# Kernel tuning notes

Hardware: AMD Instinct MI355X
Metric: run time of the kernel (lower is better)

Reference implementation:

```python
import jax, jax.numpy as jnp
import numpy as np

N, E, H = 5000, 40000, 8
DIMS = [(258, 512), (516, 256), (262, 128), (136, 20)]  # (in_feature, out_feature) per GATDeformer


def setup_inputs() -> dict:
    key = jax.random.key(0)
    ks = jax.random.split(key, 10)
    s = 0.05
    data = jax.random.normal(ks[0], (N, 10), jnp.float32)
    src = jax.random.randint(ks[1], (E,), 0, N)
    off = jax.random.randint(ks[2], (E,), 1, N)
    edge_idx = jnp.stack([src, (src + off) % N]).astype(jnp.int32)  # no self loops by construction
    inp = {
        'data': data,
        'edge_idx': edge_idx,
        'W0': jax.random.normal(ks[3], (10, 256), jnp.float32) * s,
        'b0': jnp.zeros((256,), jnp.float32),
    }
    for i, (din, dout) in enumerate(DIMS, start=1):
        k = jax.random.split(ks[3 + i], 3)
        inp[f'W{i}'] = jax.random.normal(k[0], (din, H * dout), jnp.float32) * s
        inp[f'asrc{i}'] = jax.random.normal(k[1], (H, dout), jnp.float32) * s
        inp[f'adst{i}'] = jax.random.normal(k[2], (H, dout), jnp.float32) * s
        inp[f'bias{i}'] = jnp.zeros((dout,), jnp.float32)
    return inp


def _gat(x, src, dst, W, a_s, a_d, b):
    """PyG GATConv (concat=False): returns (mean-over-heads output + bias, alpha [E',H])."""
    Hh, C = a_s.shape
    h = (x @ W).reshape(N, Hh, C)                               # [N,H,C]
    e_s = jnp.einsum('nhc,hc->nh', h, a_s)                      # [N,H]
    e_d = jnp.einsum('nhc,hc->nh', h, a_d)
    logits = jax.nn.leaky_relu(e_s[src] + e_d[dst], 0.2)        # [E',H]
    m = jax.ops.segment_max(logits, dst, num_segments=N)        # segment softmax over incoming edges
    ex = jnp.exp(logits - m[dst])
    alpha = ex / jax.ops.segment_sum(ex, dst, num_segments=N)[dst]
    out = jax.ops.segment_sum(alpha[:, :, None] * h[src], dst, num_segments=N)  # [N,H,C]
    return out.mean(axis=1) + b, alpha


def _deformer(af, src, dst, W, a_s, a_d, b):
    # find_boundary on the layer input features
    up, down = af[:, 0] == 1.0, af[:, 0] == 0.0
    left, right = af[:, 1] == 0.0, af[:, 1] == 1.0
    feat, alpha = _gat(af, src, dst, W, a_s, a_d, b)
    coord = af[:, :2]
    # second propagate: alpha*0.2 reused to aggregate source coordinates, then mean over heads
    msg = (alpha * 0.2)[:, :, None] * coord[src][:, None, :]    # [E',H,2]
    oc = jax.ops.segment_sum(msg, dst, num_segments=N).mean(axis=1)
    # fix_boundary (sequential overwrite order: up then down, left then right)
    c0 = jnp.where(down, 0.0, jnp.where(up, 1.0, oc[:, 0]))
    c1 = jnp.where(right, 1.0, jnp.where(left, 0.0, oc[:, 1]))
    return jnp.stack([c0, c1], axis=1), jax.nn.selu(feat)


def reference(data, edge_idx, W0, b0, W1, asrc1, adst1, bias1, W2, asrc2, adst2, bias2, W3, asrc3, adst3, bias3, W4, asrc4, adst4, bias4):
    sl = jnp.arange(N, dtype=edge_idx.dtype)
    src = jnp.concatenate([edge_idx[0], sl])   # GATConv add_self_loops=True
    dst = jnp.concatenate([edge_idx[1], sl])
    coord = data[:, :2]
    feat = jax.nn.selu(data @ W0 + b0)
    c1_, f1 = _deformer(jnp.concatenate([coord, feat], 1), src, dst, W1, asrc1, adst1, bias1)
    c2_, f2 = _deformer(jnp.concatenate([c1_, coord, f1], 1), src, dst, W2, asrc2, adst2, bias2)
    c3_, f3 = _deformer(jnp.concatenate([c2_, c1_, coord, f2], 1), src, dst, W3, asrc3, adst3, bias3)
    c4_, _ = _deformer(jnp.concatenate([c3_, c2_, c1_, coord, f3], 1), src, dst, W4, asrc4, adst4, bias4)
    return c4_
```

## Files before the change

### kernel.cpp

```cpp
#include <hip/hip_runtime.h>

#define N_NODES 5000
#define NH 8

typedef unsigned short u16;
typedef short bf16x8 __attribute__((ext_vector_type(8)));
typedef float f32x4 __attribute__((ext_vector_type(4)));

static __device__ __forceinline__ float selu_f(float x) {
    const float sc = 1.0507009873554805f;
    const float al = 1.6732632423543772f;
    return x > 0.f ? sc * x : sc * al * (__expf(x) - 1.f);
}

static __device__ __forceinline__ u16 f2bf(float x) {
    union { float f; unsigned u; } v; v.f = x;
    unsigned r = v.u + 0x7fff + ((v.u >> 16) & 1);
    return (u16)(r >> 16);
}

static __device__ __forceinline__ float bf2f(unsigned hi16) {
    union { unsigned u; float f; } v; v.u = hi16 << 16;
    return v.f;
}

#define GL2LDS16(gp, lp)                                                        \
    __builtin_amdgcn_global_load_lds(                                           \
        (const __attribute__((address_space(1))) void*)(gp),                    \
        (__attribute__((address_space(3))) void*)(lp), 16, 0, 0)

#define WAVE_LDS_FENCE() asm volatile("s_waitcnt lgkmcnt(0)" ::: "memory")

__global__ void k_count(const int* __restrict__ ei, int* cnt, int E, int Esz) {
    int e = blockIdx.x * 256 + threadIdx.x;
    if (e >= Esz) return;
    int dst = (e < E) ? ei[E + e] : (e - E);
    atomicAdd(&cnt[dst], 1);
}

__global__ void k_scan(const int* __restrict__ cnt, int* __restrict__ rowp, int n) {
    __shared__ int ps[256];
    int t = threadIdx.x;
    int per = (n + 255) / 256;
    int b = t * per;
    int s = 0;
    for (int i = 0; i < per; ++i) { int idx = b + i; if (idx < n) s += cnt[idx]; }
    ps[t] = s;
    __syncthreads();
    for (int off = 1; off < 256; off <<= 1) {
        int v = (t >= off) ? ps[t - off] : 0;
        __syncthreads();
        ps[t] += v;
        __syncthreads();
    }
    int run = (t == 0) ? 0 : ps[t - 1];
    for (int i = 0; i < per; ++i) {
        int idx = b + i;
        if (idx < n) { rowp[idx] = run; run += cnt[idx]; }
    }
    if (t == 255) rowp[n] = run;
}

__global__ void k_fill(const int* __restrict__ ei, const int* __restrict__ rowp,
                       int* cur, int* ssrc, int E, int Esz) {
    int e = blockIdx.x * 256 + threadIdx.x;
    if (e >= Esz) return;
    int src, dst;
    if (e < E) { src = ei[e]; dst = ei[E + e]; }
    else       { src = e - E; dst = src; }
    int pos = rowp[dst] + atomicAdd(&cur[dst], 1);
    ssrc[pos] = src;
}

__global__ __launch_bounds__(256) void k_prep(
        const float* W1, const float* W2, const float* W3, const float* W4,
        const float* s1, const float* s2, const float* s3, const float* s4,
        const float* d1, const float* d2, const float* d3, const float* d4,
        float* __restrict__ fsAll, float* __restrict__ fdAll,
        u16* T1, u16* T2, u16* T3) {
    const int Ks[4] = {258, 516, 262, 136};
    const int Cs[4] = {512, 256, 128, 20};
    int bid = blockIdx.x;
    if (bid < 516) {
        int li = bid / 129;
        int k = (bid % 129) * 4 + (threadIdx.x >> 6);
        int lane = threadIdx.x & 63;
        if (k >= Ks[li]) return;
        const float* W  = (li == 0) ? W1 : (li == 1) ? W2 : (li == 2) ? W3 : W4;
        const float* as = (li == 0) ? s1 : (li == 1) ? s2 : (li == 2) ? s3 : s4;
        const float* ad = (li == 0) ? d1 : (li == 1) ? d2 : (li == 2) ? d3 : d4;
        int C = Cs[li];
        float s[8] = {0.f,0.f,0.f,0.f,0.f,0.f,0.f,0.f};
        float d[8] = {0.f,0.f,0.f,0.f,0.f,0.f,0.f,0.f};
        const float* wr = W + (size_t)k * 8 * C;
        for (int c = lane; c < C; c += 64) {
            #pragma unroll
            for (int h = 0; h < 8; ++h) {
                float w = wr[h * C + c];
                s[h] += w * as[h * C + c];
                d[h] += w * ad[h * C + c];
            }
        }
        #pragma unroll
        for (int off = 32; off >= 1; off >>= 1) {
            #pragma unroll
            for (int h = 0; h < 8; ++h) {
                s[h] += __shfl_xor(s[h], off);
                d[h] += __shfl_xor(d[h], off);
            }
        }
        if (lane == 0) {
            float* fo = fsAll + (size_t)li * 516 * 8 + k * 8;
            float* go = fdAll + (size_t)li * 516 * 8 + k * 8;
            #pragma unroll
            for (int h = 0; h < 8; ++h) { fo[h] = s[h]; go[h] = d[h]; }
        }
    } else {
        const int Kps[3] = {288, 544, 288};
        int w = bid - 516;
        int li = w / (16 * 136);
        int rem = w % (16 * 136);
        int c0 = (rem % 16) * 32;
        int j0 = (rem / 16) * 32;
        int C = Cs[li], K = Ks[li], Kp = Kps[li], KK = 8 * Kp;
        if (c0 >= C || j0 >= KK) return;
        const float* W = (li == 0) ? W1 : (li == 1) ? W2 : W3;
        u16* Wt2 = (li == 0) ? T1 : (li == 1) ? T2 : T3;
        __shared__ float tile[32][33];
        int h = j0 / Kp, k0 = j0 % Kp;
        int tid = threadIdx.x;
        for (int idx = tid; idx < 1024; idx += 256) {
            int kr = idx >> 5, cc = idx & 31;
            int gk = k0 + kr;
            tile[kr][cc] = (gk < K) ? W[(size_t)gk * (8 * C) + h * C + c0 + cc] : 0.f;
        }
        __syncthreads();
        for (int idx = tid; idx < 1024; idx += 256) {
            int cr = idx >> 5, kc = idx & 31;
            Wt2[(size_t)(c0 + cr) * KK + j0 + kc] = f2bf(tile[kc][cr]);
        }
    }
}

__global__ __launch_bounds__(256) void k_mf(const float* p0, const float* p1,
                                            const float* p2, const float* p3, int np,
                                            const float* __restrict__ data,
                                            const float* __restrict__ W0,
                                            const float* __restrict__ b0,
                                            const u16* __restrict__ facc,
                                            const float* __restrict__ biasp,
                                            int split, int MN, int FC, int K, int Kp,
                                            const float* __restrict__ fs,
                                            const float* __restrict__ fd,
                                            u16* __restrict__ afb,
                                            float* __restrict__ es, float* __restrict__ ed,
                                            float* __restrict__ c0out) {
    int n = blockIdx.x, t = threadIdx.x;
    __shared__ float drow[10];
    bool l1 = (biasp == nullptr);
    if (l1 && t < 10) drow[t] = data[n * 10 + t];
    __syncthreads();
    float pes[8] = {0.f,0.f,0.f,0.f,0.f,0.f,0.f,0.f};
    float ped[8] = {0.f,0.f,0.f,0.f,0.f,0.f,0.f,0.f};
    u16* rowb = afb + (size_t)n * Kp;
    for (int cf2 = t; 2 * cf2 < FC; cf2 += 256) {
        int cf = 2 * cf2;
        float v0, v1;
        if (l1) {
            float2 bb = *(const float2*)(b0 + cf);
            v0 = bb.x; v1 = bb.y;
            #pragma unroll
            for (int k = 0; k < 10; ++k) {
                float2 ww = *(const float2*)(W0 + k * 256 + cf);
                v0 += drow[k] * ww.x;
                v1 += drow[k] * ww.y;
            }
            v0 = selu_f(v0); v1 = selu_f(v1);
        } else {
            float s0 = 0.f, s1 = 0.f;
            for (int z = 0; z < split; ++z) {
                unsigned pr = *(const unsigned*)(facc + (size_t)z * MN + (size_t)n * FC + cf);
                s0 += bf2f(pr & 0xffff);
                s1 += bf2f(pr >> 16);
            }
            float2 bb = *(const float2*)(biasp + cf);
            v0 = selu_f(s0 * 0.125f + bb.x);
            v1 = selu_f(s1 * 0.125f + bb.y);
        }
        int c = 2 * np + cf;
        *(unsigned*)(rowb + c) = (unsigned)f2bf(v0) | ((unsigned)f2bf(v1) << 16);
        const float* fsr = fs + c * 8;
        const float* fdr = fd + c * 8;
        #pragma unroll
        for (int h = 0; h < 8; ++h) {
            pes[h] += v0 * fsr[h] + v1 * fsr[8 + h];
            ped[h] += v0 * fdr[h] + v1 * fdr[8 + h];
        }
    }
    if (t < 2 * np) {
        float v;
        if (l1) {
            v = drow[t];
            c0out[n * 2 + t] = v;
        } else {
            const float* p = (t < 2) ? p0 : (t < 4) ? p1 : (t < 6) ? p2 : p3;
            v = p[n * 2 + (t & 1)];
        }
        rowb[t] = f2bf(v);
        #pragma unroll
        for (int h = 0; h < 8; ++h) { pes[h] += v * fs[t * 8 + h]; ped[h] += v * fd[t * 8 + h]; }
    }
    for (int c = K + t; c < Kp; c += 256) rowb[c] = 0;
    #pragma unroll
    for (int off = 32; off >= 1; off >>= 1) {
        #pragma unroll
        for (int h = 0; h < 8; ++h) {
            pes[h] += __shfl_xor(pes[h], off);
            ped[h] += __shfl_xor(ped[h], off);
        }
    }
    __shared__ float red[4][16];
    int wv = t >> 6, ln = t & 63;
    if (ln == 0) {
        #pragma unroll
        for (int h = 0; h < 8; ++h) { red[wv][h] = pes[h]; red[wv][8 + h] = ped[h]; }
    }
    __syncthreads();
    if (t < 16) {
        float s = red[0][t] + red[1][t] + red[2][t] + red[3][t];
        if (t < 8) es[n * 8 + t] = s;
        else       ed[n * 8 + (t - 8)] = s;
    }
}

template <int S>
__global__ __launch_bounds__(256) void k_gag2(const float* __restrict__ es,
                            const float* __restrict__ ed,
                            const int* __restrict__ rowp, const int* __restrict__ ssrc,
                            const float* __restrict__ cprev, const u16* __restrict__ afb,
                            u16* __restrict__ g, float* __restrict__ cnext, int Kp) {
    __shared__ float la_s[4][128 * 8];
    __shared__ int   ls_s[4][128];
    __shared__ float linv_s[4][8];
    int w4 = threadIdx.x >> 6, lane = threadIdx.x & 63;
    int n = blockIdx.x * 4 + w4;
    if (n >= N_NODES) return;
    float* la = la_s[w4];
    int*   ls = ls_s[w4];
    float* linv = linv_s[w4];

    int s0 = rowp[n];
    int deg = rowp[n + 1] - s0;
    if (deg > 128) deg = 128;
    for (int i = lane; i < deg; i += 64) ls[i] = ssrc[s0 + i];
    WAVE_LDS_FENCE();

    int h = lane & 7, ei = lane >> 3;
    float edh = ed[n * 8 + h];
    float m = -1e30f;
    for (int b = 0; b < deg; b += 8) {
        int e = b + ei;
        if (e < deg) {
            float x = es[ls[e] * 8 + h] + edh;
            x = x > 0.f ? x : 0.2f * x;
            la[e * 8 + h] = x;
            m = fmaxf(m, x);
        }
    }
    m = fmaxf(m, __shfl_xor(m, 8));
    m = fmaxf(m, __shfl_xor(m, 16));
    m = fmaxf(m, __shfl_xor(m, 32));
    WAVE_LDS_FENCE();
    float ssum = 0.f;
    for (int b = 0; b < deg; b += 8) {
        int e = b + ei;
        if (e < deg) {
            float v = __expf(la[e * 8 + h] - m);
            la[e * 8 + h] = v;
            ssum += v;
        }
    }
    ssum += __shfl_xor(ssum, 8);
    ssum += __shfl_xor(ssum, 16);
    ssum += __shfl_xor(ssum, 32);
    if (lane < 8) linv[lane] = 1.f / ssum;
    WAVE_LDS_FENCE();

    int nW = Kp >> 1;
    float linv8[8];
    #pragma unroll
// ... 165 lines not shown
    }
#undef STAGE_T
    u16* out = facc16 + (size_t)z * MN;
    #pragma unroll
    for (int mi = 0; mi < 4; ++mi) {
        int row0s = bm + wm + mi * 16 + q * 4;
        #pragma unroll
        for (int ni = 0; ni < 4; ++ni) {
            int col = bn + wn + ni * 16 + l16;
            #pragma unroll
            for (int r = 0; r < 4; ++r) {
                int row = row0s + r;
                if (row < M) out[(size_t)row * NC + col] = f2bf(acc[mi][ni][r]);
            }
        }
    }
}

__global__ void k_final(const float* __restrict__ es, const float* __restrict__ ed,
                        const int* __restrict__ rowp, const int* __restrict__ ssrc,
                        const float* __restrict__ cprev, float* __restrict__ outp) {
    int wid = (blockIdx.x * blockDim.x + threadIdx.x) >> 6;
    int lane = threadIdx.x & 63;
    if (wid >= N_NODES) return;
    int n = wid;
    int s0 = rowp[n], deg = rowp[n + 1] - s0;
    int h = lane & 7, ei = lane >> 3;
    float edh = ed[n * 8 + h];
    float m = -1e30f;
    for (int b = 0; b < deg; b += 8) {
        int e = b + ei;
        if (e < deg) {
            int src = ssrc[s0 + e];
            float x = es[src * 8 + h] + edh;
            x = x > 0.f ? x : 0.2f * x;
            m = fmaxf(m, x);
        }
    }
    m = fmaxf(m, __shfl_xor(m, 8));
    m = fmaxf(m, __shfl_xor(m, 16));
    m = fmaxf(m, __shfl_xor(m, 32));
    float ssum = 0.f;
    for (int b = 0; b < deg; b += 8) {
        int e = b + ei;
        if (e < deg) {
            int src = ssrc[s0 + e];
            float x = es[src * 8 + h] + edh;
            x = x > 0.f ? x : 0.2f * x;
            ssum += __expf(x - m);
        }
    }
    ssum += __shfl_xor(ssum, 8);
    ssum += __shfl_xor(ssum, 16);
    ssum += __shfl_xor(ssum, 32);
    float inv = 1.f / ssum;
    float oc0 = 0.f, oc1 = 0.f;
    for (int b = 0; b < deg; b += 8) {
        int e = b + ei;
        if (e < deg) {
            int src = ssrc[s0 + e];
            float x = es[src * 8 + h] + edh;
            x = x > 0.f ? x : 0.2f * x;
            float w = __expf(x - m) * inv;
            w += __shfl_xor(w, 1);
            w += __shfl_xor(w, 2);
            w += __shfl_xor(w, 4);
            if (h == 0) {
                oc0 += w * cprev[src * 2];
                oc1 += w * cprev[src * 2 + 1];
            }
        }
    }
    oc0 += __shfl_xor(oc0, 8);  oc1 += __shfl_xor(oc1, 8);
    oc0 += __shfl_xor(oc0, 16); oc1 += __shfl_xor(oc1, 16);
    oc0 += __shfl_xor(oc0, 32); oc1 += __shfl_xor(oc1, 32);
    if (lane == 0) {
        oc0 *= 0.025f; oc1 *= 0.025f;
        float a0 = cprev[n * 2], a1 = cprev[n * 2 + 1];
        outp[n * 2]     = (a0 == 0.f) ? 0.f : ((a0 == 1.f) ? 1.f : oc0);
        outp[n * 2 + 1] = (a1 == 1.f) ? 1.f : ((a1 == 0.f) ? 0.f : oc1);
    }
}

extern "C" void kernel_launch(void* const* d_in, const int* in_sizes, int n_in,
                              void* d_out, int out_size, void* d_ws, size_t ws_size,
                              hipStream_t stream) {
    const float* data = (const float*)d_in[0];
    const int* ei = (const int*)d_in[1];
    const float* W0 = (const float*)d_in[2];
    const float* b0 = (const float*)d_in[3];
    int E = in_sizes[1] / 2;
    int Esz = E + N_NODES;

    char* wp = (char*)d_ws;
    size_t off = 0;
    auto alloc = [&](size_t bytes) {
        void* p = wp + off;
        off += (bytes + 1023) & ~(size_t)1023;
        return p;
    };
    u16*   g     = (u16*)alloc((size_t)N_NODES * 8 * 576 * 2);
    u16*   T1    = (u16*)alloc((size_t)512 * 8 * 288 * 2);
    u16*   T2    = (u16*)alloc((size_t)256 * 8 * 544 * 2);
    u16*   T3    = (u16*)alloc((size_t)128 * 8 * 288 * 2);
    u16*   facc  = (u16*)alloc((size_t)8 * N_NODES * 512 * 2);
    u16*   afb   = (u16*)alloc((size_t)N_NODES * 576 * 2);
    float* es    = (float*)alloc((size_t)N_NODES * 8 * 4);
    float* ebd   = (float*)alloc((size_t)N_NODES * 8 * 4);
    float* fsAll = (float*)alloc((size_t)4 * 516 * 8 * 4);
    float* fdAll = (float*)alloc((size_t)4 * 516 * 8 * 4);
    float* c0    = (float*)alloc(N_NODES * 2 * 4);
    float* c1    = (float*)alloc(N_NODES * 2 * 4);
    float* c2    = (float*)alloc(N_NODES * 2 * 4);
    float* c3    = (float*)alloc(N_NODES * 2 * 4);
    int* cnt  = (int*)alloc(N_NODES * 2 * 4);
    int* cur  = cnt + N_NODES;
    int* rowp = (int*)alloc((N_NODES + 1) * 4);
    int* ssrc = (int*)alloc(Esz * 4);

    hipMemsetAsync(cnt, 0, N_NODES * 2 * 4, stream);
    int gE = (Esz + 255) / 256;
    k_count<<<gE, 256, 0, stream>>>(ei, cnt, E, Esz);
    k_scan<<<1, 256, 0, stream>>>(cnt, rowp, N_NODES);
    k_fill<<<gE, 256, 0, stream>>>(ei, rowp, cur, ssrc, E, Esz);

    struct LP { const float *W, *as, *ad, *bs; int K, C, split; };
    LP L[4] = {
        {(const float*)d_in[4],  (const float*)d_in[5],  (const float*)d_in[6],  (const float*)d_in[7],  258, 512, 4},
        {(const float*)d_in[8],  (const float*)d_in[9],  (const float*)d_in[10], (const float*)d_in[11], 516, 256, 8},
        {(const float*)d_in[12], (const float*)d_in[13], (const float*)d_in[14], (const float*)d_in[15], 262, 128, 8},
        {(const float*)d_in[16], (const float*)d_in[17], (const float*)d_in[18], (const float*)d_in[19], 136, 20, 1},
    };
    k_prep<<<516 + 16 * 136 * 3, 256, 0, stream>>>(
        L[0].W, L[1].W, L[2].W, L[3].W,
        L[0].as, L[1].as, L[2].as, L[3].as,
        L[0].ad, L[1].ad, L[2].ad, L[3].ad,
        fsAll, fdAll, T1, T2, T3);

    float* cbuf[4] = {c0, c1, c2, c3};
    u16* Tb[3] = {T1, T2, T3};
    int FC[4] = {256, 512, 256, 128};

    for (int li = 0; li < 4; ++li) {
        LP& lp = L[li];
        const float* p[4] = {nullptr, nullptr, nullptr, nullptr};
        for (int j = 0; j <= li; ++j) p[j] = cbuf[li - j];
        int Kp = ((lp.K + 31) / 32) * 32;
        int KK = 8 * Kp;
        const float* biasp = (li == 0) ? nullptr : L[li - 1].bs;
        int splitp = (li == 0) ? 1 : L[li - 1].split;
        int MNp = N_NODES * FC[li];
        const float* fs = fsAll + (size_t)li * 516 * 8;
        const float* fd = fdAll + (size_t)li * 516 * 8;

        k_mf<<<N_NODES, 256, 0, stream>>>(p[0], p[1], p[2], p[3], li + 1,
                                          data, W0, b0, facc, biasp, splitp, MNp, FC[li],
                                          lp.K, Kp, fs, fd, afb, es, ebd, c0);
        if (li < 3) {
            int gG = (N_NODES + 3) / 4;
            if (Kp == 544)
                k_gag2<5><<<gG, 256, 0, stream>>>(es, ebd, rowp, ssrc, cbuf[li], afb,
                                                  g, cbuf[li + 1], Kp);
            else
                k_gag2<3><<<gG, 256, 0, stream>>>(es, ebd, rowp, ssrc, cbuf[li], afb,
                                                  g, cbuf[li + 1], Kp);
            int MN = N_NODES * lp.C;
            k_gemm_s<<<dim3(lp.C / 128, (N_NODES + 127) / 128, lp.split), 256, 0, stream>>>(
                g, Tb[li], facc, N_NODES, KK, lp.C, KK / lp.split, MN);
        } else {
            k_final<<<(N_NODES + 3) / 4, 256, 0, stream>>>(es, ebd, rowp, ssrc, cbuf[3],
                                                           (float*)d_out);
        }
    }
}
```

Before: 359.3 us.

## Fuse entire GAT network into one persistent cooperative kernel with grid syncs

Replaces the sequence of separate kernel launches (CSR build, weight prep, per-layer feature build, gather-aggregate, GEMM, final coordinate pass) with a single cooperative persistent kernel that separates phases with grid-wide barriers. This removes launch overhead and inter-kernel gaps across the roughly dozen dependent stages. In exchange, occupancy is capped at 2 blocks per CU via launch bounds, the shared-memory union sizes every phase to the largest one, and each grid.sync adds its own barrier latency. The old multi-kernel path is kept as a fallback if the cooperative launch fails.

```diff
diff --git a/kernel.cpp b/kernel.cpp
--- a/kernel.cpp
+++ b/kernel.cpp
@@ -1,4 +1,7 @@
 #include <hip/hip_runtime.h>
+#include <hip/hip_cooperative_groups.h>
+
+namespace cg = cooperative_groups;
 
 #define N_NODES 5000
 #define NH 8
@@ -30,6 +33,7 @@
         (__attribute__((address_space(3))) void*)(lp), 16, 0, 0)
 
 #define WAVE_LDS_FENCE() asm volatile("s_waitcnt lgkmcnt(0)" ::: "memory")
+
 
 __global__ void k_count(const int* __restrict__ ei, int* cnt, int E, int Esz) {
     int e = blockIdx.x * 256 + threadIdx.x;
@@ -537,6 +541,543 @@
     }
 }
 
+
+union SmemU {
+    struct { u16 As[3][4096]; u16 Bs[3][4096]; } gm;
+    struct { float la[4][1024]; int ls[4][128]; float linv[4][8]; } gg;
+    struct { float drow[10]; float red[4][16]; } mf;
+    struct { int ps[256]; } sc;
+    struct { float tile[32][33]; } pr;
+};
+
+struct NetArgs {
+    const float* data; const int* ei;
+    const float* W0; const float* b0;
+    const float* W[4]; const float* asv[4]; const float* adv[4]; const float* bsv[4];
+    float* fsAll; float* fdAll;
+    u16* T1; u16* T2; u16* T3;
+    u16* g; u16* facc; u16* afb;
+    float* es; float* ebd;
+    float* c0; float* c1; float* c2; float* c3;
+    float* outp;
+    int* cnt; int* curp; int* rowp; int* ssrc;
+    int E, Esz;
+};
+
+template <int S>
+__device__ __forceinline__ void gag_phase(const NetArgs& a, const float* cprev,
+                                          float* cnext, int Kp, SmemU& sm, int NBLK) {
+    int w4 = threadIdx.x >> 6, lane = threadIdx.x & 63;
+    float* la = sm.gg.la[w4];
+    int*   ls = sm.gg.ls[w4];
+    float* linv = sm.gg.linv[w4];
+    const int NB4 = (N_NODES + 3) / 4;
+    for (int nb = blockIdx.x; nb < NB4; nb += NBLK) {
+        int n = nb * 4 + w4;
+        if (n >= N_NODES) continue;
+        int s0 = a.rowp[n];
+        int deg = a.rowp[n + 1] - s0;
+        if (deg > 128) deg = 128;
+        for (int i = lane; i < deg; i += 64) ls[i] = a.ssrc[s0 + i];
+        WAVE_LDS_FENCE();
+        int h = lane & 7, ei = lane >> 3;
+        float edh = a.ebd[n * 8 + h];
+        float m = -1e30f;
+        for (int b = 0; b < deg; b += 8) {
+            int e = b + ei;
+            if (e < deg) {
+                float x = a.es[ls[e] * 8 + h] + edh;
+                x = x > 0.f ? x : 0.2f * x;
+                la[e * 8 + h] = x;
+                m = fmaxf(m, x);
+            }
+        }
+        m = fmaxf(m, __shfl_xor(m, 8));
+        m = fmaxf(m, __shfl_xor(m, 16));
+        m = fmaxf(m, __shfl_xor(m, 32));
+        WAVE_LDS_FENCE();
+        float ssum = 0.f;
+        for (int b = 0; b < deg; b += 8) {
+            int e = b + ei;
+            if (e < deg) {
+                float v = __expf(la[e * 8 + h] - m);
+                la[e * 8 + h] = v;
+                ssum += v;
+            }
+        }
+        ssum += __shfl_xor(ssum, 8);
+        ssum += __shfl_xor(ssum, 16);
+        ssum += __shfl_xor(ssum, 32);
+        if (lane < 8) linv[lane] = 1.f / ssum;
+        WAVE_LDS_FENCE();
+
+        int nW = Kp >> 1;
+        float linv8[8];
+        #pragma unroll
+        for (int h2 = 0; h2 < 8; ++h2) linv8[h2] = linv[h2];
+
+        float acc[8][2 * S];
+        #pragma unroll
+        for (int h2 = 0; h2 < 8; ++h2)
+            #pragma unroll
+            for (int s = 0; s < 2 * S; ++s) acc[h2][s] = 0.f;
+        int e = 0;
+        for (; e + 3 < deg; e += 4) {
+            const unsigned* r0 = (const unsigned*)(a.afb + (size_t)ls[e] * Kp);
+            const unsigned* r1 = (const unsigned*)(a.afb + (size_t)ls[e + 1] * Kp);
+            const unsigned* r2 = (const unsigned*)(a.afb + (size_t)ls[e + 2] * Kp);
+            const unsigned* r3 = (const unsigned*)(a.afb + (size_t)ls[e + 3] * Kp);
+            unsigned v0[S], v1[S], v2[S], v3[S];
+            #pragma unroll
+            for (int s = 0; s < S; ++s) {
+                int w = lane + 64 * s;
+                bool ok = (w < nW);
+                v0[s] = ok ? r0[w] : 0u;
+                v1[s] = ok ? r1[w] : 0u;
+                v2[s] = ok ? r2[w] : 0u;
+                v3[s] = ok ? r3[w] : 0u;
+            }
+            float a0[8], a1[8], a2[8], a3[8];
+            #pragma unroll
+            for (int h2 = 0; h2 < 8; ++h2) {
+                a0[h2] = la[(e + 0) * 8 + h2];
+                a1[h2] = la[(e + 1) * 8 + h2];
+                a2[h2] = la[(e + 2) * 8 + h2];
+                a3[h2] = la[(e + 3) * 8 + h2];
+            }
+            #pragma unroll
+            for (int s = 0; s < S; ++s) {
+                float x0 = bf2f(v0[s] & 0xffff), y0 = bf2f(v0[s] >> 16);
+                float x1 = bf2f(v1[s] & 0xffff), y1 = bf2f(v1[s] >> 16);
+                float x2 = bf2f(v2[s] & 0xffff), y2 = bf2f(v2[s] >> 16);
+                float x3 = bf2f(v3[s] & 0xffff), y3 = bf2f(v3[s] >> 16);
+                #pragma unroll
+                for (int h2 = 0; h2 < 8; ++h2) {
+                    acc[h2][2 * s]     += a0[h2] * x0 + a1[h2] * x1 + a2[h2] * x2 + a3[h2] * x3;
+                    acc[h2][2 * s + 1] += a0[h2] * y0 + a1[h2] * y1 + a2[h2] * y2 + a3[h2] * y3;
+                }
+            }
+        }
+        for (; e < deg; ++e) {
+            const unsigned* r0 = (const unsigned*)(a.afb + (size_t)ls[e] * Kp);
+            unsigned v0[S];
+            #pragma unroll
+            for (int s = 0; s < S; ++s) {
+                int w = lane + 64 * s;
+                v0[s] = (w < nW) ? r0[w] : 0u;
+            }
+            float a0[8];
+            #pragma unroll
+            for (int h2 = 0; h2 < 8; ++h2) a0[h2] = la[e * 8 + h2];
+            #pragma unroll
+            for (int s = 0; s < S; ++s) {
+                float x0 = bf2f(v0[s] & 0xffff), y0 = bf2f(v0[s] >> 16);
+                #pragma unroll
+                for (int h2 = 0; h2 < 8; ++h2) {
+                    acc[h2][2 * s]     += a0[h2] * x0;
+                    acc[h2][2 * s + 1] += a0[h2] * y0;
+                }
+            }
+        }
+        unsigned* grw = (unsigned*)(a.g + (size_t)n * 8 * Kp);
+        #pragma unroll
+        for (int s = 0; s < S; ++s) {
+            int w = lane + 64 * s;
+            if (w < nW) {
+                #pragma unroll
+                for (int h2 = 0; h2 < 8; ++h2) {
+                    float iv = linv8[h2];
+                    unsigned lo = f2bf(acc[h2][2 * s] * iv);
+                    unsigned hi = f2bf(acc[h2][2 * s + 1] * iv);
+                    grw[h2 * nW + w] = lo | (hi << 16);
+                }
+            }
+        }
+        float oc0 = 0.f, oc1 = 0.f;
+        for (int i = lane; i < deg; i += 64) {
+            float wsum = 0.f;
+            #pragma unroll
+            for (int h2 = 0; h2 < 8; ++h2) wsum += la[i * 8 + h2] * linv8[h2];
+            int src = ls[i];
+            oc0 += wsum * cprev[src * 2];
+            oc1 += wsum * cprev[src * 2 + 1];
+        }
+        #pragma unroll
+        for (int off = 1; off <= 32; off <<= 1) {
+            oc0 += __shfl_xor(oc0, off);
+            oc1 += __shfl_xor(oc1, off);
+        }
+        if (lane == 0) {
+            oc0 *= 0.025f; oc1 *= 0.025f;
+            float a0 = cprev[n * 2], a1 = cprev[n * 2 + 1];
+            cnext[n * 2]     = (a0 == 0.f) ? 0.f : ((a0 == 1.f) ? 1.f : oc0);
+            cnext[n * 2 + 1] = (a1 == 1.f) ? 1.f : ((a1 == 0.f) ? 0.f : oc1);
+        }
+    }
+}
+
+__global__ __launch_bounds__(256, 2) void k_net(NetArgs a) {
+    __shared__ SmemU sm;
+    cg::grid_group grd = cg::this_grid();
+    const int NBLK = gridDim.x;
+    const int tid = threadIdx.x;
+    const int bid = blockIdx.x;
+
+    for (int i = bid * 256 + tid; i < 2 * N_NODES; i += NBLK * 256) a.cnt[i] = 0;
+    grd.sync();
+    for (int e = bid * 256 + tid; e < a.Esz; e += NBLK * 256) {
+        int dst = (e < a.E) ? a.ei[a.E + e] : (e - a.E);
+        atomicAdd(&a.cnt[dst], 1);
+    }
+    grd.sync();
+    if (bid == 0) {
+        int t = tid;
+        int per = (N_NODES + 255) / 256;
+        int b = t * per;
+        int s = 0;
+        for (int i = 0; i < per; ++i) { int idx = b + i; if (idx < N_NODES) s += a.cnt[idx]; }
+        sm.sc.ps[t] = s;
+        __syncthreads();
+        for (int off = 1; off < 256; off <<= 1) {
+            int v = (t >= off) ? sm.sc.ps[t - off] : 0;
+            __syncthreads();
+            sm.sc.ps[t] += v;
+            __syncthreads();
+        }
+        int run = (t == 0) ? 0 : sm.sc.ps[t - 1];
+        for (int i = 0; i < per; ++i) {
+            int idx = b + i;
+            if (idx < N_NODES) { a.rowp[idx] = run; run += a.cnt[idx]; }
+        }
+        if (t == 255) a.rowp[N_NODES] = run;
+    }
+    grd.sync();
+    for (int e = bid * 256 + tid; e < a.Esz; e += NBLK * 256) {
+        int src, dst;
+        if (e < a.E) { src = a.ei[e]; dst = a.ei[a.E + e]; }
+        else         { src = e - a.E; dst = src; }
+        int pos = a.rowp[dst] + atomicAdd(&a.curp[dst], 1);
+        a.ssrc[pos] = src;
+    }
+    grd.sync();
+    {
+        const int Ks[4] = {258, 516, 262, 136};
+        const int Cs[4] = {512, 256, 128, 20};
+        const int NPREP = 516 + 16 * 136 * 3;
+        for (int vb = bid; vb < NPREP; vb += NBLK) {
+            if (vb < 516) {
+                int li = vb / 129;
+                int k = (vb % 129) * 4 + (tid >> 6);
+                int lane = tid & 63;
+                if (k < Ks[li]) {
+                    const float* W  = a.W[li];
+                    const float* as = a.asv[li];
+                    const float* ad = a.adv[li];
+                    int C = Cs[li];
+                    float s[8] = {0.f,0.f,0.f,0.f,0.f,0.f,0.f,0.f};
+                    float d[8] = {0.f,0.f,0.f,0.f,0.f,0.f,0.f,0.f};
+                    const float* wr = W + (size_t)k * 8 * C;
+                    for (int c = lane; c < C; c += 64) {
+                        #pragma unroll
+                        for (int h = 0; h < 8; ++h) {
+                            float w = wr[h * C + c];
+                            s[h] += w * as[h * C + c];
+                            d[h] += w * ad[h * C + c];
+                        }
+                    }
+                    #pragma unroll
+                    for (int off = 32; off >= 1; off >>= 1) {
+                        #pragma unroll
+                        for (int h = 0; h < 8; ++h) {
+                            s[h] += __shfl_xor(s[h], off);
+                            d[h] += __shfl_xor(d[h], off);
+                        }
+                    }
+                    if (lane == 0) {
+                        float* fo = a.fsAll + (size_t)li * 516 * 8 + k * 8;
+                        float* go = a.fdAll + (size_t)li * 516 * 8 + k * 8;
+                        #pragma unroll
+                        for (int h = 0; h < 8; ++h) { fo[h] = s[h]; go[h] = d[h]; }
+                    }
+                }
+            } else {
+                const int Kps[3] = {288, 544, 288};
+                int w = vb - 516;
+                int li = w / (16 * 136);
+                int rem = w % (16 * 136);
+                int c0 = (rem % 16) * 32;
+                int j0 = (rem / 16) * 32;
+                int C = Cs[li], K = Ks[li], Kp = Kps[li], KK = 8 * Kp;
+                if (c0 < C && j0 < KK) {
+                    const float* W = (li == 0) ? a.W[0] : (li == 1) ? a.W[1] : a.W[2];
+                    u16* Wt2 = (li == 0) ? a.T1 : (li == 1) ? a.T2 : a.T3;
+                    int h = j0 / Kp, k0 = j0 % Kp;
+                    for (int idx = tid; idx < 1024; idx += 256) {
+                        int kr = idx >> 5, cc = idx & 31;
+                        int gk = k0 + kr;
+                        sm.pr.tile[kr][cc] = (gk < K) ? W[(size_t)gk * (8 * C) + h * C + c0 + cc] : 0.f;
+                    }
+                    __syncthreads();
+                    for (int idx = tid; idx < 1024; idx += 256) {
+                        int cr = idx >> 5, kc = idx & 31;
+                        Wt2[(size_t)(c0 + cr) * KK + j0 + kc] = f2bf(sm.pr.tile[kc][cr]);
+                    }
+                    __syncthreads();
+                }
+            }
+        }
+    }
+    grd.sync();
+
+    const int KsL[4] = {258, 516, 262, 136};
+    const int CsL[4] = {512, 256, 128, 20};
+    const int FCs[4] = {256, 512, 256, 128};
+    const int SPL[4] = {4, 8, 8, 1};
+    float* cb[4] = {a.c0, a.c1, a.c2, a.c3};
+    for (int li = 0; li < 4; ++li) {
+        int K = KsL[li], Kp = ((K + 31) / 32) * 32, KK = 8 * Kp, FC = FCs[li];
+        const float* biasp = (li == 0) ? (const float*)nullptr : a.bsv[li - 1];
+        int splitp = (li == 0) ? 1 : SPL[li - 1];
+        int MNp = N_NODES * FC;
+        const float* fs = a.fsAll + (size_t)li * 516 * 8;
+        const float* fd = a.fdAll + (size_t)li * 516 * 8;
+        const float* p0 = cb[li];
+        const float* p1 = (li >= 1) ? cb[li - 1] : (const float*)nullptr;
+        const float* p2 = (li >= 2) ? cb[li - 2] : (const float*)nullptr;
+        const float* p3 = (li >= 3) ? cb[li - 3] : (const float*)nullptr;
+        int np = li + 1;
+        bool l1 = (li == 0);
+
+        for (int n = bid; n < N_NODES; n += NBLK) {
+            int t = tid;
+            if (l1 && t < 10) sm.mf.drow[t] = a.data[n * 10 + t];
+            __syncthreads();
+            float pes[8] = {0.f,0.f,0.f,0.f,0.f,0.f,0.f,0.f};
+            float ped[8] = {0.f,0.f,0.f,0.f,0.f,0.f,0.f,0.f};
+            u16* rowb = a.afb + (size_t)n * Kp;
+            for (int cf2 = t; 2 * cf2 < FC; cf2 += 256) {
+                int cf = 2 * cf2;
+                float v0, v1;
+                if (l1) {
+                    float2 bb = *(const float2*)(a.b0 + cf);
+                    v0 = bb.x; v1 = bb.y;
+                    #pragma unroll
+                    for (int k = 0; k < 10; ++k) {
+                        float2 ww = *(const float2*)(a.W0 + k * 256 + cf);
+                        v0 += sm.mf.drow[k] * ww.x;
+                        v1 += sm.mf.drow[k] * ww.y;
+                    }
+                    v0 = selu_f(v0); v1 = selu_f(v1);
+                } else {
+                    float s0 = 0.f, s1 = 0.f;
+                    for (int z = 0; z < splitp; ++z) {
+                        unsigned pr = *(const unsigned*)(a.facc + (size_t)z * MNp + (size_t)n * FC + cf);
+                        s0 += bf2f(pr & 0xffff);
+                        s1 += bf2f(pr >> 16);
+                    }
+                    float2 bb = *(const float2*)(biasp + cf);
+                    v0 = selu_f(s0 * 0.125f + bb.x);
+                    v1 = selu_f(s1 * 0.125f + bb.y);
+                }
+                int c = 2 * np + cf;
+                *(unsigned*)(rowb + c) = (unsigned)f2bf(v0) | ((unsigned)f2bf(v1) << 16);
+                const float* fsr = fs + c * 8;
+                const float* fdr = fd + c * 8;
+                #pragma unroll
+                for (int h = 0; h < 8; ++h) {
+                    pes[h] += v0 * fsr[h] + v1 * fsr[8 + h];
+                    ped[h] += v0 * fdr[h] + v1 * fdr[8 + h];
+                }
+            }
+            if (t < 2 * np) {
+                float v;
+                if (l1) {
+                    v = sm.mf.drow[t];
+                    a.c0[n * 2 + t] = v;
+                } else {
+                    const float* p = (t < 2) ? p0 : (t < 4) ? p1 : (t < 6) ? p2 : p3;
+                    v = p[n * 2 + (t & 1)];
+                }
+                rowb[t] = f2bf(v);
+                #pragma unroll
+                for (int h = 0; h < 8; ++h) { pes[h] += v * fs[t * 8 + h]; ped[h] += v * fd[t * 8 + h]; }
+            }
+            for (int c = K + t; c < Kp; c += 256) rowb[c] = 0;
+            #pragma unroll
+            for (int off = 32; off >= 1; off >>= 1) {
+                #pragma unroll
+                for (int h = 0; h < 8; ++h) {
+                    pes[h] += __shfl_xor(pes[h], off);
+                    ped[h] += __shfl_xor(ped[h], off);
+                }
+            }
+            int wv = t >> 6, ln = t & 63;
+            if (ln == 0) {
+                #pragma unroll
+                for (int h = 0; h < 8; ++h) { sm.mf.red[wv][h] = pes[h]; sm.mf.red[wv][8 + h] = ped[h]; }
+            }
+            __syncthreads();
+            if (t < 16) {
+                float s = sm.mf.red[0][t] + sm.mf.red[1][t] + sm.mf.red[2][t] + sm.mf.red[3][t];
+                if (t < 8) a.es[n * 8 + t] = s;
+                else       a.ebd[n * 8 + (t - 8)] = s;
+            }
+            __syncthreads();
+        }
+        grd.sync();
+
+        if (li < 3) {
+            if (Kp == 544) gag_phase<5>(a, cb[li], cb[li + 1], Kp, sm, NBLK);
+            else           gag_phase<3>(a, cb[li], cb[li + 1], Kp, sm, NBLK);
+            grd.sync();
+            {
+                int split = SPL[li], NC = CsL[li];
+                int nbx = NC / 128, nby = (N_NODES + 127) / 128;
+                int ntile = nbx * nby * split;
+                int kchunk = KK / split, MN = N_NODES * NC;
+                const u16* A = a.g;
+                const u16* Bt = (li == 0) ? a.T1 : (li == 1) ? a.T2 : a.T3;
+                int wave = tid >> 6, lane = tid & 63;
+                int wm = (wave >> 1) * 64, wn = (wave & 1) * 64;
+                int l16 = lane & 15, q = lane >> 4;
+                int seg0 = wave * 128 + lane;
+                int seg1 = seg0 + 64;
+                int row0 = seg0 >> 2, sq0 = (seg0 & 3) ^ (row0 & 3);
+                int row1 = seg1 >> 2, sq1 = (seg1 & 3) ^ (row1 & 3);
+                int lo0 = (wave * 2 + 0) * 512;
+                int lo1 = (wave * 2 + 1) * 512;
+                for (int tl = bid; tl < ntile; tl += NBLK) {
+                    int bx = tl % nbx, r2 = tl / nbx;
+                    int by = r2 % nby, z = r2 / nby;
+                    int bm = by * 128, bn = bx * 128;
+                    int kbeg = z * kchunk, kend = kbeg + kchunk;
+                    if (kend > KK) kend = KK;
+                    const u16* ga0 = A  + (size_t)(bm + row0) * KK + sq0 * 8;
+                    const u16* ga1 = A  + (size_t)(bm + row1) * KK + sq1 * 8;
+                    const u16* gb0 = Bt + (size_t)(bn + row0) * KK + sq0 * 8;
+                    const u16* gb1 = Bt + (size_t)(bn + row1) * KK + sq1 * 8;
+                    auto STAGE = [&](int buf, int kk) {
+                        GL2LDS16(ga0 + kk, &sm.gm.As[buf][lo0]);
+                        GL2LDS16(ga1 + kk, &sm.gm.As[buf][lo1]);
+                        GL2LDS16(gb0 + kk, &sm.gm.Bs[buf][lo0]);
+                        GL2LDS16(gb1 + kk, &sm.gm.Bs[buf][lo1]);
+                    };
+                    f32x4 acc[4][4] = {};
+                    STAGE(0, kbeg);
+                    if (kbeg + 32 < kend) STAGE(1, kbeg + 32);
+                    int cur = 0;
+                    for (int k0 = kbeg; k0 < kend; k0 += 32) {
+                        if (k0 + 64 < kend) {
+                            int nbuf = cur + 2; if (nbuf >= 3) nbuf -= 3;
+                            STAGE(nbuf, k0 + 64);
+                            asm volatile("s_waitcnt vmcnt(8)" ::: "memory");
+                        } else if (k0 + 32 < kend) {
+                            asm volatile("s_waitcnt vmcnt(4)" ::: "memory");
+                        } else {
+                            asm volatile("s_waitcnt vmcnt(0)" ::: "memory");
+                        }
+                        __builtin_amdgcn_s_barrier();
+                        const u16* Asr = sm.gm.As[cur];
+                        const u16* Bsr = sm.gm.Bs[cur];
+                        bf16x8 fa[4], fb[4];
+                        #pragma unroll
+                        for (int mi = 0; mi < 4; ++mi) {
+                            int row = wm + mi * 16 + l16;
+                            fa[mi] = *(const bf16x8*)(Asr + row * 32 + ((q ^ (row & 3)) * 8));
+                            int col = wn + mi * 16 + l16;
+                            fb[mi] = *(const bf16x8*)(Bsr + col * 32 + ((q ^ (col & 3)) * 8));
+                        }
+                        #pragma unroll
+                        for (int mi = 0; mi < 4; ++mi)
+                            #pragma unroll
+                            for (int ni = 0; ni < 4; ++ni)
+                                acc[mi][ni] = __builtin_amdgcn_mfma_f32_16x16x32_bf16(fa[mi], fb[ni], acc[mi][ni], 0, 0, 0);
+                        __builtin_amdgcn_s_barrier();
+                        cur += 1; if (cur >= 3) cur -= 3;
+                    }
+                    u16* out = a.facc + (size_t)z * MN;
+                    #pragma unroll
+                    for (int mi = 0; mi < 4; ++mi) {
+                        int row0s = bm + wm + mi * 16 + q * 4;
+                        #pragma unroll
+                        for (int ni = 0; ni < 4; ++ni) {
+                            int col = bn + wn + ni * 16 + l16;
+                            #pragma unroll
+                            for (int r = 0; r < 4; ++r) {
+                                int row = row0s + r;
+                                if (row < N_NODES) out[(size_t)row * NC + col] = f2bf(acc[mi][ni][r]);
+                            }
+                        }
+                    }
+                }
+            }
+            grd.sync();
+        } else {
+            int w4 = tid >> 6, lane = tid & 63;
+            const float* cprev = cb[3];
+            for (int n = bid * 4 + w4; n < N_NODES; n += NBLK * 4) {
+                int s0 = a.rowp[n], deg = a.rowp[n + 1] - s0;
+                int h = lane & 7, ei = lane >> 3;
+                float edh = a.ebd[n * 8 + h];
+                float m = -1e30f;
+                for (int b = 0; b < deg; b += 8) {
+                    int e = b + ei;
+                    if (e < deg) {
+                        int src = a.ssrc[s0 + e];
+                        float x = a.es[src * 8 + h] + edh;
+                        x = x > 0.f ? x : 0.2f * x;
+                        m = fmaxf(m, x);
+                    }
+                }
+                m = fmaxf(m, __shfl_xor(m, 8));
+                m = fmaxf(m, __shfl_xor(m, 16));
+                m = fmaxf(m, __shfl_xor(m, 32));
+                float ssum = 0.f;
+                for (int b = 0; b < deg; b += 8) {
+                    int e = b + ei;
+                    if (e < deg) {
+                        int src = a.ssrc[s0 + e];
+                        float x = a.es[src * 8 + h] + edh;
+                        x = x > 0.f ? x : 0.2f * x;
+                        ssum += __expf(x - m);
+                    }
+                }
+                ssum += __shfl_xor(ssum, 8);
+                ssum += __shfl_xor(ssum, 16);
+                ssum += __shfl_xor(ssum, 32);
+                float inv = 1.f / ssum;
+                float oc0 = 0.f, oc1 = 0.f;
+                for (int b = 0; b < deg; b += 8) {
+                    int e = b + ei;
+                    if (e < deg) {
+                        int src = a.ssrc[s0 + e];
+                        float x = a.es[src * 8 + h] + edh;
+                        x = x > 0.f ? x : 0.2f * x;
+                        float w = __expf(x - m) * inv;
+                        w += __shfl_xor(w, 1);
+                        w += __shfl_xor(w, 2);
+                        w += __shfl_xor(w, 4);
+                        if (h == 0) {
+                            oc0 += w * cprev[src * 2];
+                            oc1 += w * cprev[src * 2 + 1];
+                        }
+                    }
+                }
+                oc0 += __shfl_xor(oc0, 8);  oc1 += __shfl_xor(oc1, 8);
+                oc0 += __shfl_xor(oc0, 16); oc1 += __shfl_xor(oc1, 16);
+                oc0 += __shfl_xor(oc0, 32); oc1 += __shfl_xor(oc1, 32);
+                if (lane == 0) {
+                    oc0 *= 0.025f; oc1 *= 0.025f;
+                    float a0 = cprev[n * 2], a1 = cprev[n * 2 + 1];
+                    a.outp[n * 2]     = (a0 == 0.f) ? 0.f : ((a0 == 1.f) ? 1.f : oc0);
+                    a.outp[n * 2 + 1] = (a1 == 1.f) ? 1.f : ((a1 == 0.f) ? 0.f : oc1);
+                }
+            }
+        }
+    }
+}
+
+
 extern "C" void kernel_launch(void* const* d_in, const int* in_sizes, int n_in,
                               void* d_out, int out_size, void* d_ws, size_t ws_size,
                               hipStream_t stream) {
@@ -573,12 +1114,6 @@
     int* rowp = (int*)alloc((N_NODES + 1) * 4);
     int* ssrc = (int*)alloc(Esz * 4);
 
-    hipMemsetAsync(cnt, 0, N_NODES * 2 * 4, stream);
-    int gE = (Esz + 255) / 256;
-    k_count<<<gE, 256, 0, stream>>>(ei, cnt, E, Esz);
-    k_scan<<<1, 256, 0, stream>>>(cnt, rowp, N_NODES);
-    k_fill<<<gE, 256, 0, stream>>>(ei, rowp, cur, ssrc, E, Esz);
-
     struct LP { const float *W, *as, *ad, *bs; int K, C, split; };
     LP L[4] = {
         {(const float*)d_in[4],  (const float*)d_in[5],  (const float*)d_in[6],  (const float*)d_in[7],  258, 512, 4},
@@ -586,6 +1121,49 @@
         {(const float*)d_in[12], (const float*)d_in[13], (const float*)d_in[14], (const float*)d_in[15], 262, 128, 8},
         {(const float*)d_in[16], (const float*)d_in[17], (const float*)d_in[18], (const float*)d_in[19], 136, 20, 1},
     };
+
+    static int coopGrid = -1;
+    if (coopGrid < 0) {
+        int bpc = 0;
+        if (hipOccupancyMaxActiveBlocksPerMultiprocessor(&bpc, k_net, 256, 0) != hipSuccess)
+            bpc = 0;
+        int nCU = 256;
+        hipDeviceProp_t prop;
+        int dev = 0;
+        if (hipGetDevice(&dev) == hipSuccess &&
+            hipGetDeviceProperties(&prop, dev) == hipSuccess &&
+            prop.multiProcessorCount > 0)
+            nCU = prop.multiProcessorCount;
+        coopGrid = bpc * nCU;
+        if (coopGrid > 2048) coopGrid = 2048;
+    }
+
+    hipError_t cerr = hipErrorUnknown;
+    if (coopGrid >= 64) {
+        NetArgs a;
+        a.data = data; a.ei = ei; a.W0 = W0; a.b0 = b0;
+        for (int i = 0; i < 4; ++i) {
+            a.W[i] = L[i].W; a.asv[i] = L[i].as; a.adv[i] = L[i].ad; a.bsv[i] = L[i].bs;
+        }
+        a.fsAll = fsAll; a.fdAll = fdAll;
+        a.T1 = T1; a.T2 = T2; a.T3 = T3;
+        a.g = g; a.facc = facc; a.afb = afb;
+        a.es = es; a.ebd = ebd;
+        a.c0 = c0; a.c1 = c1; a.c2 = c2; a.c3 = c3;
+        a.outp = (float*)d_out;
+        a.cnt = cnt; a.curp = cur; a.rowp = rowp; a.ssrc = ssrc;
+        a.E = E; a.Esz = Esz;
+        void* kargs[] = { (void*)&a };
+        cerr = hipLaunchCooperativeKernel(k_net, dim3(coopGrid), dim3(256), kargs, 0, stream);
+    }
+    if (cerr == hipSuccess) return;
+
+    hipMemsetAsync(cnt, 0, N_NODES * 2 * 4, stream);
+    int gE = (Esz + 255) / 256;
+    k_count<<<gE, 256, 0, stream>>>(ei, cnt, E, Esz);
+    k_scan<<<1, 256, 0, stream>>>(cnt, rowp, N_NODES);
+    k_fill<<<gE, 256, 0, stream>>>(ei, rowp, cur, ssrc, E, Esz);
+
     k_prep<<<516 + 16 * 136 * 3, 256, 0, stream>>>(
         L[0].W, L[1].W, L[2].W, L[3].W,
         L[0].as, L[1].as, L[2].as, L[3].as,
```

Measured after the change: 1.022 ms. 185% more time.

## Fold CSR build into prep and layer-1 feature kernels to cut launches

Applied to the files above, without the earlier changes.

Removes the memset, count, scan and fill kernels. The degree histogram and prefix scan now run in one extra block of the weight-prep kernel using a shared-memory histogram (self-loops are counted by initialising it to 1). The CSR fill is merged into a new layer-1 feature kernel that also computes the initial SELU features. This trims launch and serialization overhead across the graph-building stage. In exchange, every prep block now reserves about 20KB of shared memory, which may lower occupancy, and the scan runs serially in a single block.

```diff
diff --git a/kernel.cpp b/kernel.cpp
--- a/kernel.cpp
+++ b/kernel.cpp
@@ -31,55 +31,19 @@
 
 #define WAVE_LDS_FENCE() asm volatile("s_waitcnt lgkmcnt(0)" ::: "memory")
 
-__global__ void k_count(const int* __restrict__ ei, int* cnt, int E, int Esz) {
-    int e = blockIdx.x * 256 + threadIdx.x;
-    if (e >= Esz) return;
-    int dst = (e < E) ? ei[E + e] : (e - E);
-    atomicAdd(&cnt[dst], 1);
-}
-
-__global__ void k_scan(const int* __restrict__ cnt, int* __restrict__ rowp, int n) {
-    __shared__ int ps[256];
-    int t = threadIdx.x;
-    int per = (n + 255) / 256;
-    int b = t * per;
-    int s = 0;
-    for (int i = 0; i < per; ++i) { int idx = b + i; if (idx < n) s += cnt[idx]; }
-    ps[t] = s;
-    __syncthreads();
-    for (int off = 1; off < 256; off <<= 1) {
-        int v = (t >= off) ? ps[t - off] : 0;
-        __syncthreads();
-        ps[t] += v;
-        __syncthreads();
-    }
-    int run = (t == 0) ? 0 : ps[t - 1];
-    for (int i = 0; i < per; ++i) {
-        int idx = b + i;
-        if (idx < n) { rowp[idx] = run; run += cnt[idx]; }
-    }
-    if (t == 255) rowp[n] = run;
-}
-
-__global__ void k_fill(const int* __restrict__ ei, const int* __restrict__ rowp,
-                       int* cur, int* ssrc, int E, int Esz) {
-    int e = blockIdx.x * 256 + threadIdx.x;
-    if (e >= Esz) return;
-    int src, dst;
-    if (e < E) { src = ei[e]; dst = ei[E + e]; }
-    else       { src = e - E; dst = src; }
-    int pos = rowp[dst] + atomicAdd(&cur[dst], 1);
-    ssrc[pos] = src;
-}
-
-__global__ __launch_bounds__(256) void k_prep(
+__global__ __launch_bounds__(256) void k_prepcs(
         const float* W1, const float* W2, const float* W3, const float* W4,
         const float* s1, const float* s2, const float* s3, const float* s4,
         const float* d1, const float* d2, const float* d3, const float* d4,
         float* __restrict__ fsAll, float* __restrict__ fdAll,
-        u16* T1, u16* T2, u16* T3) {
+        u16* T1, u16* T2, u16* T3,
+        const int* __restrict__ ei, int E,
+        int* __restrict__ rowp, int* __restrict__ curp) {
     const int Ks[4] = {258, 516, 262, 136};
     const int Cs[4] = {512, 256, 128, 20};
+    __shared__ float tile[32][33];
+    __shared__ int hist[N_NODES];
+    __shared__ int ps2[256];
     int bid = blockIdx.x;
     if (bid < 516) {
         int li = bid / 129;
@@ -115,7 +79,7 @@
             #pragma unroll
             for (int h = 0; h < 8; ++h) { fo[h] = s[h]; go[h] = d[h]; }
         }
-    } else {
+    } else if (bid < 7044) {
         const int Kps[3] = {288, 544, 288};
         int w = bid - 516;
         int li = w / (16 * 136);
@@ -126,7 +90,6 @@
         if (c0 >= C || j0 >= KK) return;
         const float* W = (li == 0) ? W1 : (li == 1) ? W2 : W3;
         u16* Wt2 = (li == 0) ? T1 : (li == 1) ? T2 : T3;
-        __shared__ float tile[32][33];
         int h = j0 / Kp, k0 = j0 % Kp;
         int tid = threadIdx.x;
         for (int idx = tid; idx < 1024; idx += 256) {
@@ -139,54 +102,136 @@
             int cr = idx >> 5, kc = idx & 31;
             Wt2[(size_t)(c0 + cr) * KK + j0 + kc] = f2bf(tile[kc][cr]);
         }
+    } else {
+        int t = threadIdx.x;
+        for (int i = t; i < N_NODES; i += 256) hist[i] = 1;
+        __syncthreads();
+        for (int e = t; e < E; e += 256) atomicAdd(&hist[ei[E + e]], 1);
+        __syncthreads();
+        int per = (N_NODES + 255) / 256;
+        int b = t * per;
+        int s = 0;
+        for (int i = 0; i < per; ++i) { int idx = b + i; if (idx < N_NODES) s += hist[idx]; }
+        ps2[t] = s;
+        __syncthreads();
+        for (int off = 1; off < 256; off <<= 1) {
+            int v = (t >= off) ? ps2[t - off] : 0;
+            __syncthreads();
+            ps2[t] += v;
+            __syncthreads();
+        }
+        int run = (t == 0) ? 0 : ps2[t - 1];
+        for (int i = 0; i < per; ++i) {
+            int idx = b + i;
+            if (idx < N_NODES) { rowp[idx] = run; run += hist[idx]; }
+        }
+        if (t == 255) rowp[N_NODES] = run;
+        for (int i = t; i < N_NODES; i += 256) curp[i] = 0;
+    }
+}
+
+__global__ __launch_bounds__(256) void k_fmf1(
+        const int* __restrict__ ei, const int* __restrict__ rowp,
+        int* __restrict__ curp, int* __restrict__ ssrc, int E, int Esz, int gE,
+        const float* __restrict__ data, const float* __restrict__ W0,
+        const float* __restrict__ b0,
+        const float* __restrict__ fs, const float* __restrict__ fd,
+        u16* __restrict__ afb, float* __restrict__ es, float* __restrict__ ed,
+        float* __restrict__ c0out) {
+    int bid = blockIdx.x, t = threadIdx.x;
+    if (bid < gE) {
+        int e = bid * 256 + t;
+        if (e >= Esz) return;
+        int src, dst;
+        if (e < E) { src = ei[e]; dst = ei[E + e]; }
+        else       { src = e - E; dst = src; }
+        int pos = rowp[dst] + atomicAdd(&curp[dst], 1);
+        ssrc[pos] = src;
+        return;
+    }
+    const int FC = 256, K = 258, Kp = 288;
+    int n = bid - gE;
+    __shared__ float drow[10];
+    if (t < 10) drow[t] = data[n * 10 + t];
+    __syncthreads();
+    float pes[8] = {0.f,0.f,0.f,0.f,0.f,0.f,0.f,0.f};
+    float ped[8] = {0.f,0.f,0.f,0.f,0.f,0.f,0.f,0.f};
+    u16* rowb = afb + (size_t)n * Kp;
+    for (int cf2 = t; 2 * cf2 < FC; cf2 += 256) {
+        int cf = 2 * cf2;
+        float2 bb = *(const float2*)(b0 + cf);
+        float v0 = bb.x, v1 = bb.y;
+        #pragma unroll
+        for (int k = 0; k < 10; ++k) {
+            float2 ww = *(const float2*)(W0 + k * 256 + cf);
+            v0 += drow[k] * ww.x;
+            v1 += drow[k] * ww.y;
+        }
+        v0 = selu_f(v0); v1 = selu_f(v1);
+        int c = 2 + cf;
+        *(unsigned*)(rowb + c) = (unsigned)f2bf(v0) | ((unsigned)f2bf(v1) << 16);
+        const float* fsr = fs + c * 8;
+        const float* fdr = fd + c * 8;
+        #pragma unroll
+        for (int h = 0; h < 8; ++h) {
+            pes[h] += v0 * fsr[h] + v1 * fsr[8 + h];
+            ped[h] += v0 * fdr[h] + v1 * fdr[8 + h];
+        }
+    }
+    if (t < 2) {
+        float v = drow[t];
+        c0out[n * 2 + t] = v;
+        rowb[t] = f2bf(v);
+        #pragma unroll
+        for (int h = 0; h < 8; ++h) { pes[h] += v * fs[t * 8 + h]; ped[h] += v * fd[t * 8 + h]; }
+    }
+    for (int c = K + t; c < Kp; c += 256) rowb[c] = 0;
+    #pragma unroll
+    for (int off = 32; off >= 1; off >>= 1) {
+        #pragma unroll
+        for (int h = 0; h < 8; ++h) {
+            pes[h] += __shfl_xor(pes[h], off);
+            ped[h] += __shfl_xor(ped[h], off);
+        }
+    }
+    __shared__ float red[4][16];
+    int wv = t >> 6, ln = t & 63;
+    if (ln == 0) {
+        #pragma unroll
+        for (int h = 0; h < 8; ++h) { red[wv][h] = pes[h]; red[wv][8 + h] = ped[h]; }
+    }
+    __syncthreads();
+    if (t < 16) {
+        float s = red[0][t] + red[1][t] + red[2][t] + red[3][t];
+        if (t < 8) es[n * 8 + t] = s;
+        else       ed[n * 8 + (t - 8)] = s;
     }
 }
 
 __global__ __launch_bounds__(256) void k_mf(const float* p0, const float* p1,
                                             const float* p2, const float* p3, int np,
-                                            const float* __restrict__ data,
-                                            const float* __restrict__ W0,
-                                            const float* __restrict__ b0,
                                             const u16* __restrict__ facc,
                                             const float* __restrict__ biasp,
                                             int split, int MN, int FC, int K, int Kp,
                                             const float* __restrict__ fs,
                                             const float* __restrict__ fd,
                                             u16* __restrict__ afb,
-                                            float* __restrict__ es, float* __restrict__ ed,
-                                            float* __restrict__ c0out) {
+                                            float* __restrict__ es, float* __restrict__ ed) {
     int n = blockIdx.x, t = threadIdx.x;
-    __shared__ float drow[10];
-    bool l1 = (biasp == nullptr);
-    if (l1 && t < 10) drow[t] = data[n * 10 + t];
-    __syncthreads();
     float pes[8] = {0.f,0.f,0.f,0.f,0.f,0.f,0.f,0.f};
     float ped[8] = {0.f,0.f,0.f,0.f,0.f,0.f,0.f,0.f};
     u16* rowb = afb + (size_t)n * Kp;
     for (int cf2 = t; 2 * cf2 < FC; cf2 += 256) {
         int cf = 2 * cf2;
-        float v0, v1;
-        if (l1) {
-            float2 bb = *(const float2*)(b0 + cf);
-            v0 = bb.x; v1 = bb.y;
-            #pragma unroll
-            for (int k = 0; k < 10; ++k) {
-                float2 ww = *(const float2*)(W0 + k * 256 + cf);
-                v0 += drow[k] * ww.x;
-                v1 += drow[k] * ww.y;
-            }
-            v0 = selu_f(v0); v1 = selu_f(v1);
-        } else {
-            float s0 = 0.f, s1 = 0.f;
-            for (int z = 0; z < split; ++z) {
-                unsigned pr = *(const unsigned*)(facc + (size_t)z * MN + (size_t)n * FC + cf);
-                s0 += bf2f(pr & 0xffff);
-                s1 += bf2f(pr >> 16);
-            }
-            float2 bb = *(const float2*)(biasp + cf);
-            v0 = selu_f(s0 * 0.125f + bb.x);
-            v1 = selu_f(s1 * 0.125f + bb.y);
-        }
+        float s0 = 0.f, s1 = 0.f;
+        for (int z = 0; z < split; ++z) {
+            unsigned pr = *(const unsigned*)(facc + (size_t)z * MN + (size_t)n * FC + cf);
+            s0 += bf2f(pr & 0xffff);
+            s1 += bf2f(pr >> 16);
+        }
+        float2 bb = *(const float2*)(biasp + cf);
+        float v0 = selu_f(s0 * 0.125f + bb.x);
+        float v1 = selu_f(s1 * 0.125f + bb.y);
         int c = 2 * np + cf;
         *(unsigned*)(rowb + c) = (unsigned)f2bf(v0) | ((unsigned)f2bf(v1) << 16);
         const float* fsr = fs + c * 8;
@@ -198,14 +243,8 @@
         }
     }
     if (t < 2 * np) {
-        float v;
-        if (l1) {
-            v = drow[t];
-            c0out[n * 2 + t] = v;
-        } else {
-            const float* p = (t < 2) ? p0 : (t < 4) ? p1 : (t < 6) ? p2 : p3;
-            v = p[n * 2 + (t & 1)];
-        }
+        const float* p = (t < 2) ? p0 : (t < 4) ? p1 : (t < 6) ? p2 : p3;
+        float v = p[n * 2 + (t & 1)];
         rowb[t] = f2bf(v);
         #pragma unroll
         for (int h = 0; h < 8; ++h) { pes[h] += v * fs[t * 8 + h]; ped[h] += v * fd[t * 8 + h]; }
@@ -546,6 +585,7 @@
     const float* b0 = (const float*)d_in[3];
     int E = in_sizes[1] / 2;
     int Esz = E + N_NODES;
+    int gE = (Esz + 255) / 256;
 
     char* wp = (char*)d_ws;
     size_t off = 0;
@@ -568,16 +608,9 @@
     float* c1    = (float*)alloc(N_NODES * 2 * 4);
     float* c2    = (float*)alloc(N_NODES * 2 * 4);
     float* c3    = (float*)alloc(N_NODES * 2 * 4);
-    int* cnt  = (int*)alloc(N_NODES * 2 * 4);
-    int* cur  = cnt + N_NODES;
+    int* cur  = (int*)alloc(N_NODES * 4);
     int* rowp = (int*)alloc((N_NODES + 1) * 4);
     int* ssrc = (int*)alloc(Esz * 4);
-
-    hipMemsetAsync(cnt, 0, N_NODES * 2 * 4, stream);
-    int gE = (Esz + 255) / 256;
-    k_count<<<gE, 256, 0, stream>>>(ei, cnt, E, Esz);
-    k_scan<<<1, 256, 0, stream>>>(cnt, rowp, N_NODES);
-    k_fill<<<gE, 256, 0, stream>>>(ei, rowp, cur, ssrc, E, Esz);
 
     struct LP { const float *W, *as, *ad, *bs; int K, C, split; };
     LP L[4] = {
@@ -586,11 +619,18 @@
         {(const float*)d_in[12], (const float*)d_in[13], (const float*)d_in[14], (const float*)d_in[15], 262, 128, 8},
         {(const float*)d_in[16], (const float*)d_in[17], (const float*)d_in[18], (const float*)d_in[19], 136, 20, 1},
     };
-    k_prep<<<516 + 16 * 136 * 3, 256, 0, stream>>>(
+
+    k_prepcs<<<7045, 256, 0, stream>>>(
         L[0].W, L[1].W, L[2].W, L[3].W,
         L[0].as, L[1].as, L[2].as, L[3].as,
         L[0].ad, L[1].ad, L[2].ad, L[3].ad,
-        fsAll, fdAll, T1, T2, T3);
+        fsAll, fdAll, T1, T2, T3,
+        ei, E, rowp, cur);
+
+    k_fmf1<<<gE + N_NODES, 256, 0, stream>>>(
+        ei, rowp, cur, ssrc, E, Esz, gE,
+        data, W0, b0,
+        fsAll + 0, fdAll + 0, afb, es, ebd, c0);
 
     float* cbuf[4] = {c0, c1, c2, c3};
     u16* Tb[3] = {T1, T2, T3};
@@ -598,19 +638,21 @@
 
     for (int li = 0; li < 4; ++li) {
         LP& lp = L[li];
-        const float* p[4] = {nullptr, nullptr, nullptr, nullptr};
-        for (int j = 0; j <= li; ++j) p[j] = cbuf[li - j];
         int Kp = ((lp.K + 31) / 32) * 32;
         int KK = 8 * Kp;
-        const float* biasp = (li == 0) ? nullptr : L[li - 1].bs;
-        int splitp = (li == 0) ? 1 : L[li - 1].split;
-        int MNp = N_NODES * FC[li];
-        const float* fs = fsAll + (size_t)li * 516 * 8;
-        const float* fd = fdAll + (size_t)li * 516 * 8;
-
-        k_mf<<<N_NODES, 256, 0, stream>>>(p[0], p[1], p[2], p[3], li + 1,
-                                          data, W0, b0, facc, biasp, splitp, MNp, FC[li],
-                                          lp.K, Kp, fs, fd, afb, es, ebd, c0);
+
+        if (li >= 1) {
+            const float* p[4] = {nullptr, nullptr, nullptr, nullptr};
+            for (int j = 0; j <= li; ++j) p[j] = cbuf[li - j];
+            const float* biasp = L[li - 1].bs;
+            int splitp = L[li - 1].split;
+            int MNp = N_NODES * FC[li];
+            const float* fs = fsAll + (size_t)li * 516 * 8;
+            const float* fd = fdAll + (size_t)li * 516 * 8;
+            k_mf<<<N_NODES, 256, 0, stream>>>(p[0], p[1], p[2], p[3], li + 1,
+                                              facc, biasp, splitp, MNp, FC[li],
+                                              lp.K, Kp, fs, fd, afb, es, ebd);
+        }
         if (li < 3) {
             int gG = (N_NODES + 3) / 4;
             if (Kp == 544)
```

Result: slower. 374.1 us (+4.1%).
